# Kernel optimization log

Hardware: AMD Instinct MI355X
Metric: run time of the kernel (lower is better)

Reference implementation:

```python
import jax, jax.numpy as jnp
import numpy as np
from jax import lax

DIM, HF, WF = 768, 14, 8   # h = H, w = W//2 + 1
B, H, W = 128, 14, 14
EPS = 1e-5


def setup_inputs() -> dict:
    key = jax.random.key(0)
    k = jax.random.split(key, 5)
    half = DIM // 2
    return {
        "x": jax.random.normal(k[0], (B, DIM, H, W), dtype=jnp.float32),
        "dw_weight": jax.random.normal(k[1], (half, 1, 3, 3), dtype=jnp.float32) * 0.1,
        "complex_weight": jax.random.normal(k[2], (half, HF, WF, 2), dtype=jnp.float32) * 0.02,
        "proj_weight": jax.random.normal(k[3], (DIM, DIM, 1, 1), dtype=jnp.float32) * 0.02,
        "proj_bias": jnp.zeros((DIM,), dtype=jnp.float32),
        "bn_gamma": jnp.ones((DIM,), dtype=jnp.float32),
        "bn_beta": jnp.zeros((DIM,), dtype=jnp.float32),
    }


def reference(x, dw_weight, complex_weight, proj_weight, proj_bias, bn_gamma, bn_beta):
    half = x.shape[1] // 2
    x1, x2 = x[:, :half], x[:, half:]

    # depthwise 3x3 conv, padding=1, no bias
    x1 = lax.conv_general_dilated(
        x1, dw_weight, window_strides=(1, 1), padding="SAME",
        dimension_numbers=("NCHW", "OIHW", "NCHW"), feature_group_count=half)

    # spectral filter: rfft2 -> complex elementwise multiply -> irfft2 (ortho norm)
    x2_fft = jnp.fft.rfft2(x2, norm="ortho")               # [B, half, H, W//2+1]
    w_fft = complex_weight[..., 0] + 1j * complex_weight[..., 1]  # [half, h, w]
    x2_filt = jnp.fft.irfft2(x2_fft * w_fft, s=(x2.shape[-2], x2.shape[-1]), norm="ortho")

    out = jnp.concatenate((x1, x2_filt), axis=1)           # [B, DIM, H, W]

    # 1x1 projection conv with bias (a GEMM over channels)
    w = proj_weight[:, :, 0, 0]                            # [DIM, DIM]
    out = jnp.einsum("bchw,oc->bohw", out, w) + proj_bias[None, :, None, None]

    # BatchNorm2d, training mode (batch statistics over N,H,W)
    mean = jnp.mean(out, axis=(0, 2, 3), keepdims=True)
    var = jnp.var(out, axis=(0, 2, 3), keepdims=True)
    out = (out - mean) * lax.rsqrt(var + EPS)
    out = out * bn_gamma[None, :, None, None] + bn_beta[None, :, None, None]
    return out
```

## Files before the change

kernel.cpp:

```cpp
#include <hip/hip_runtime.h>

typedef __attribute__((ext_vector_type(8))) __bf16 bf16x8;
typedef __attribute__((ext_vector_type(4))) float f32x4;

#define B_    128
#define DIM_  768
#define HALF_ 384
#define HW_   196
#define NPOS_ (B_*HW_)
#define IMG_  (DIM_*HW_)

__device__ __forceinline__ unsigned short f2bf(float f) {
  unsigned int u = __builtin_bit_cast(unsigned int, f);
  u = (u + 0x7FFFu + ((u >> 16) & 1u)) >> 16;
  return (unsigned short)u;
}

__global__ void k_wspatial(const float* __restrict__ cw, float* __restrict__ wsp) {
  __shared__ float ct[14], st[14];
  const int c = blockIdx.x;
  const int tid = threadIdx.x;
  if (tid < 14) {
    float s, co;
    sincosf(0.44879895051282760549f * (float)tid, &s, &co);
    ct[tid] = co; st[tid] = s;
  }
  __syncthreads();
  const int y = tid / 14, xx = tid % 14;
  float acc = 0.f;
  for (int u = 0; u < 14; ++u) {
    #pragma unroll
    for (int v = 0; v < 8; ++v) {
      int idx = (u * y + v * xx) % 14;
      float wr = cw[(((size_t)c * 14 + u) * 8 + v) * 2 + 0];
      float wi = cw[(((size_t)c * 14 + u) * 8 + v) * 2 + 1];
      float fac = (v == 0 || v == 7) ? 1.f : 2.f;
      acc += fac * (wr * ct[idx] - wi * st[idx]);
    }
  }
  wsp[(size_t)c * 196 + tid] = acc * (1.f / 196.f);
}

__global__ void k_cvtW(const float* __restrict__ pw, unsigned short* __restrict__ Wb) {
  int i = blockIdx.x * 256 + threadIdx.x;
  float4 v = reinterpret_cast<const float4*>(pw)[i];
  unsigned int lo = (unsigned int)f2bf(v.x) | ((unsigned int)f2bf(v.y) << 16);
  unsigned int hi = (unsigned int)f2bf(v.z) | ((unsigned int)f2bf(v.w) << 16);
  reinterpret_cast<uint2*>(Wb)[i] = make_uint2(lo, hi);
}

__global__ __launch_bounds__(256) void k_dwconv(
    const float* __restrict__ x, const float* __restrict__ dww,
    unsigned short* __restrict__ featT) {
  __shared__ __align__(16) float xin[16][196];
  __shared__ float wgt[16][9];
  __shared__ __align__(16) unsigned short outT[196][16];
  const int cgrp = blockIdx.x;
  const int b = blockIdx.y;
  const int c0 = cgrp * 16;
  const int tid = threadIdx.x;

  for (int i = tid; i < 16 * 196; i += 256)
    xin[i / 196][i % 196] = x[(size_t)b * IMG_ + (size_t)(c0 + i / 196) * 196 + (i % 196)];
  if (tid < 144) wgt[tid / 9][tid % 9] = dww[(size_t)c0 * 9 + tid];
  __syncthreads();

  if (tid < 224) {
    const int cc = tid / 14;
    const int y0 = tid % 14;
    float w00 = wgt[cc][0], w01 = wgt[cc][1], w02 = wgt[cc][2];
    float w10 = wgt[cc][3], w11 = wgt[cc][4], w12 = wgt[cc][5];
    float w20 = wgt[cc][6], w21 = wgt[cc][7], w22 = wgt[cc][8];
    #pragma unroll
    for (int xx = 0; xx < 14; ++xx) {
      float acc = 0.f;
      #pragma unroll
      for (int ky = 0; ky < 3; ++ky) {
        int yy = y0 + ky - 1;
        bool yok = (yy >= 0) && (yy <= 13);
        #pragma unroll
        for (int kx = 0; kx < 3; ++kx) {
          int xs = xx + kx - 1;
          if (xs < 0 || xs > 13) continue;
          float wv = (ky == 0) ? (kx == 0 ? w00 : kx == 1 ? w01 : w02)
                   : (ky == 1) ? (kx == 0 ? w10 : kx == 1 ? w11 : w12)
                               : (kx == 0 ? w20 : kx == 1 ? w21 : w22);
          if (yok) acc += xin[cc][yy * 14 + xs] * wv;
        }
      }
      outT[y0 * 14 + xx][cc] = f2bf(acc);
    }
  }
  __syncthreads();
  for (int i = tid; i < 196 * 16; i += 256) {
    int pix = i >> 4, cc = i & 15;
    featT[(size_t)(b * 196 + pix) * DIM_ + (c0 + cc)] = outT[pix][cc];
  }
}

__global__ __launch_bounds__(256) void k_circconv(
    const float* __restrict__ x, const float* __restrict__ wsp,
    unsigned short* __restrict__ featT) {
  __shared__ __align__(16) float xin[16][196];
  __shared__ __align__(16) float wf[16][196];
  __shared__ __align__(16) unsigned short outT[196][16];
  const int cgrp = blockIdx.x;
  const int b = blockIdx.y;
  const int cw0 = cgrp * 16;
  const int c0 = HALF_ + cw0;
  const int tid = threadIdx.x;

  for (int i = tid; i < 16 * 196; i += 256) {
    int cc = i / 196, p = i % 196;
    xin[cc][p] = x[(size_t)b * IMG_ + (size_t)(c0 + cc) * 196 + p];
    wf[cc][p] = wsp[(size_t)(cw0 + cc) * 196 + p];
  }
  __syncthreads();

  if (tid < 224) {
    const int cc = tid / 14;
    const int y0 = tid % 14;
    float outv[14];
    #pragma unroll
    for (int i = 0; i < 14; ++i) outv[i] = 0.f;
    for (int p = 0; p < 14; ++p) {
      int ry = y0 - p; if (ry < 0) ry += 14;
      float xr[14];
      const float2* row2 = reinterpret_cast<const float2*>(&xin[cc][ry * 14]);
      #pragma unroll
      for (int j = 0; j < 7; ++j) { float2 t = row2[j]; xr[2 * j] = t.x; xr[2 * j + 1] = t.y; }
      #pragma unroll
      for (int q = 0; q < 14; ++q) {
        float wv = wf[cc][p * 14 + q];
        #pragma unroll
        for (int xo = 0; xo < 14; ++xo)
          outv[xo] += wv * xr[(xo - q + 14) % 14];
      }
    }
    #pragma unroll
    for (int xo = 0; xo < 14; ++xo) outT[y0 * 14 + xo][cc] = f2bf(outv[xo]);
  }
  __syncthreads();
  for (int i = tid; i < 196 * 16; i += 256) {
    int pix = i >> 4, cc = i & 15;
    featT[(size_t)(b * 196 + pix) * DIM_ + (c0 + cc)] = outT[pix][cc];
  }
}

__global__ __launch_bounds__(256) void k_gemm(
    const unsigned short* __restrict__ Wb, const unsigned short* __restrict__ featT,
    const float* __restrict__ bias, float* __restrict__ y) {
  __shared__ __align__(16) unsigned short As[128 * 64];
  __shared__ __align__(16) unsigned short Bs[128 * 64];

  const int bx = blockIdx.x;
  const int by = blockIdx.y;
  const int tid = threadIdx.x;
  const int lane = tid & 63;
  const int wave = tid >> 6;
  const int wm = wave >> 1;
  const int wn = wave & 1;
  const int o_blk = by * 128;
  const int n_blk = bx * 128;

  f32x4 acc[4][4];
  #pragma unroll
  for (int i = 0; i < 4; ++i)
    #pragma unroll
    for (int j = 0; j < 4; ++j) acc[i][j] = (f32x4)0.0f;

  for (int kt = 0; kt < 768; kt += 64) {
    #pragma unroll
    for (int i = 0; i < 4; ++i) {
      int chunk = i * 256 + tid;
      int r = chunk >> 3;
      int cs = (chunk & 7) * 8;
      uint4 va = *reinterpret_cast<const uint4*>(Wb + (size_t)(o_blk + r) * 768 + kt + cs);
      uint4 vb = *reinterpret_cast<const uint4*>(featT + (size_t)(n_blk + r) * 768 + kt + cs);
      *reinterpret_cast<uint4*>(&As[chunk * 8]) = va;
      *reinterpret_cast<uint4*>(&Bs[chunk * 8]) = vb;
    }
    __syncthreads();
    #pragma unroll
    for (int ks = 0; ks < 64; ks += 32) {
      bf16x8 af[4], bfr[4];
      #pragma unroll
      for (int mi = 0; mi < 4; ++mi) {
        int row = wm * 64 + mi * 16 + (lane & 15);
        int col = ks + (lane >> 4) * 8;
        af[mi] = *reinterpret_cast<const bf16x8*>(&As[row * 64 + col]);
      }
      #pragma unroll
      for (int ni = 0; ni < 4; ++ni) {
        int row = wn * 64 + ni * 16 + (lane & 15);
        int col = ks + (lane >> 4) * 8;
        bfr[ni] = *reinterpret_cast<const bf16x8*>(&Bs[row * 64 + col]);
      }
      #pragma unroll
      for (int mi = 0; mi < 4; ++mi)
        #pragma unroll
        for (int ni = 0; ni < 4; ++ni)
          acc[mi][ni] = __builtin_amdgcn_mfma_f32_16x16x32_bf16(af[mi], bfr[ni], acc[mi][ni], 0, 0, 0);
    }
    __syncthreads();
  }

  const int col_l = lane & 15;
  #pragma unroll
  for (int mi = 0; mi < 4; ++mi) {
    const int o0 = o_blk + wm * 64 + mi * 16 + (lane >> 4) * 4;
    float bs0 = bias[o0], bs1 = bias[o0 + 1], bs2 = bias[o0 + 2], bs3 = bias[o0 + 3];
    #pragma unroll
    for (int ni = 0; ni < 4; ++ni) {
      int n = n_blk + wn * 64 + ni * 16 + col_l;
      int b = n / 196;
      int hw = n % 196;
      size_t base = (size_t)b * IMG_ + (size_t)o0 * 196 + hw;
      y[base +   0] = acc[mi][ni][0] + bs0;
      y[base + 196] = acc[mi][ni][1] + bs1;
      y[base + 392] = acc[mi][ni][2] + bs2;
      y[base + 588] = acc[mi][ni][3] + bs3;
    }
  }
}

__global__ __launch_bounds__(256) void k_bnstats(const float* __restrict__ y,
                                                 float* __restrict__ stats) {
  const int o = blockIdx.x;
  const int tid = threadIdx.x;
  float s = 0.f, s2 = 0.f;
  for (int i = tid; i < NPOS_; i += 256) {
    int b = i / 196, hw = i % 196;
    float v = y[(size_t)b * IMG_ + (size_t)o * 196 + hw];
    s += v; s2 += v * v;
  }
  #pragma unroll
  for (int m = 1; m < 64; m <<= 1) { s += __shfl_xor(s, m); s2 += __shfl_xor(s2, m); }
  __shared__ float rs[4], rs2[4];
  if ((tid & 63) == 0) { rs[tid >> 6] = s; rs2[tid >> 6] = s2; }
  __syncthreads();
  if (tid == 0) {
    float S = rs[0] + rs[1] + rs[2] + rs[3];
    float S2 = rs2[0] + rs2[1] + rs2[2] + rs2[3];
    float mean = S / (float)NPOS_;
    float var = S2 / (float)NPOS_ - mean * mean;
    stats[o] = mean;
    stats[DIM_ + o] = rsqrtf(var + 1e-5f);
  }
}

__global__ void k_bnapply(float* __restrict__ y, const float* __restrict__ stats,
                          const float* __restrict__ gamma, const float* __restrict__ beta) {
  const size_t total4 = (size_t)B_ * DIM_ * HW_ / 4;
  const size_t stride = (size_t)gridDim.x * blockDim.x;
  for (size_t i4 = (size_t)blockIdx.x * blockDim.x + threadIdx.x; i4 < total4; i4 += stride) {
    float4 v = reinterpret_cast<float4*>(y)[i4];
    size_t flat = i4 * 4;
    int o = (int)((flat / 196) % DIM_);
    float g = gamma[o] * stats[DIM_ + o];
    float be = beta[o] - stats[o] * g;
    v.x = v.x * g + be; v.y = v.y * g + be; v.z = v.z * g + be; v.w = v.w * g + be;
    reinterpret_cast<float4*>(y)[i4] = v;
  }
}

extern "C" void kernel_launch(void* const* d_in, const int* in_sizes, int n_in,
                              void* d_out, int out_size, void* d_ws, size_t ws_size,
                              hipStream_t stream) {
  const float* x     = (const float*)d_in[0];
  const float* dww   = (const float*)d_in[1];
  const float* cw    = (const float*)d_in[2];
  const float* pw    = (const float*)d_in[3];
  const float* pb    = (const float*)d_in[4];
  const float* gamma = (const float*)d_in[5];
  const float* beta  = (const float*)d_in[6];
  float* out = (float*)d_out;

  char* wsb = (char*)d_ws;
  unsigned short* featT = (unsigned short*)wsb;
  unsigned short* Wb    = (unsigned short*)(wsb + 38535168);
  float* wsp   = (float*)(wsb + 38535168 + 1179648);
  float* stats = (float*)(wsb + 38535168 + 1179648 + 301056);

  k_wspatial<<<dim3(HALF_), dim3(HW_), 0, stream>>>(cw, wsp);
  k_cvtW<<<dim3(576), dim3(256), 0, stream>>>(pw, Wb);
  k_dwconv<<<dim3(24, B_), dim3(256), 0, stream>>>(x, dww, featT);
  k_circconv<<<dim3(24, B_), dim3(256), 0, stream>>>(x, wsp, featT);
  k_gemm<<<dim3(196, 6), dim3(256), 0, stream>>>(Wb, featT, pb, out);
  k_bnstats<<<dim3(DIM_), dim3(256), 0, stream>>>(out, stats);
  k_bnapply<<<dim3(2048), dim3(256), 0, stream>>>(out, stats, gamma, beta);
}
```

Before: 356.0 us.

## Run circular conv as MFMA GEMM, fuse BN stats into GEMM epilogue

The spectral branch's per-thread scalar circular convolution becomes a per-channel bf16 MFMA matmul. For each channel, a 196x196 circulant matrix built from the spatial filter multiplies the batch-by-pixel input, and a new transpose kernel writes the result back into the channel-last feature buffer. The separate BN statistics pass is removed: the GEMM epilogue reduces sum and sum of squares per channel and accumulates them with atomics, and bnapply derives mean and variance from those sums. GEMM tile loads also switch to direct global-to-LDS loads. This adds bf16 rounding of the spectral inputs, an extra intermediate buffer and transpose pass, and non-deterministic atomic accumulation.

```diff
diff --git a/kernel.cpp b/kernel.cpp
--- a/kernel.cpp
+++ b/kernel.cpp
@@ -10,10 +10,18 @@
 #define NPOS_ (B_*HW_)
 #define IMG_  (DIM_*HW_)
 
+typedef const __attribute__((address_space(1))) void* gas_t;
+typedef __attribute__((address_space(3))) void* las_t;
+
 __device__ __forceinline__ unsigned short f2bf(float f) {
   unsigned int u = __builtin_bit_cast(unsigned int, f);
   u = (u + 0x7FFFu + ((u >> 16) & 1u)) >> 16;
   return (unsigned short)u;
+}
+
+__global__ void k_zero(float* __restrict__ stats) {
+  int i = blockIdx.x * 256 + threadIdx.x;
+  if (i < 2 * DIM_) stats[i] = 0.f;
 }
 
 __global__ void k_wspatial(const float* __restrict__ cw, float* __restrict__ wsp) {
@@ -98,58 +106,114 @@
   }
 }
 
-__global__ __launch_bounds__(256) void k_circconv(
+__global__ __launch_bounds__(256) void k_circmm(
     const float* __restrict__ x, const float* __restrict__ wsp,
-    unsigned short* __restrict__ featT) {
-  __shared__ __align__(16) float xin[16][196];
-  __shared__ __align__(16) float wf[16][196];
-  __shared__ __align__(16) unsigned short outT[196][16];
-  const int cgrp = blockIdx.x;
-  const int b = blockIdx.y;
-  const int cw0 = cgrp * 16;
-  const int c0 = HALF_ + cw0;
-  const int tid = threadIdx.x;
-
-  for (int i = tid; i < 16 * 196; i += 256) {
-    int cc = i / 196, p = i % 196;
-    xin[cc][p] = x[(size_t)b * IMG_ + (size_t)(c0 + cc) * 196 + p];
-    wf[cc][p] = wsp[(size_t)(cw0 + cc) * 196 + p];
+    unsigned short* __restrict__ feat2) {
+  __shared__ __align__(16) unsigned short As[128 * 72];
+  __shared__ __align__(16) unsigned short Bs[208 * 72];
+  const int c = blockIdx.x;
+  const int tid = threadIdx.x;
+  const int lane = tid & 63;
+  const int wv = tid >> 6;
+  const int fr = lane & 15, fg = lane >> 4;
+  const float* xc = x + (size_t)(HALF_ + c) * 196;
+  const float* wspc = wsp + (size_t)c * 196;
+
+  f32x4 acc[2][13];
+  #pragma unroll
+  for (int mi = 0; mi < 2; ++mi)
+    #pragma unroll
+    for (int ni = 0; ni < 13; ++ni) acc[mi][ni] = (f32x4)0.0f;
+
+  for (int kt = 0; kt < 4; ++kt) {
+    for (int i = tid; i < 2048; i += 256) {
+      int b = i >> 4, jj = i & 15;
+      int k = kt * 64 + jj * 4;
+      ushort4 st = {0, 0, 0, 0};
+      if (k < 196) {
+        float4 v = *reinterpret_cast<const float4*>(xc + (size_t)b * IMG_ + k);
+        st.x = f2bf(v.x); st.y = f2bf(v.y); st.z = f2bf(v.z); st.w = f2bf(v.w);
+      }
+      *reinterpret_cast<ushort4*>(&As[b * 72 + jj * 4]) = st;
+    }
+    for (int i = tid; i < 12544; i += 256) {
+      int po = i >> 6, kl = i & 63;
+      int pi = kt * 64 + kl;
+      unsigned short w = 0;
+      if (pi < 196) {
+        int yo = po / 14, xo = po - yo * 14;
+        int yi = pi / 14, xi = pi - yi * 14;
+        int dy = yo - yi; dy += (dy >> 31) & 14;
+        int dx = xo - xi; dx += (dx >> 31) & 14;
+        w = f2bf(wspc[dy * 14 + dx]);
+      }
+      Bs[po * 72 + kl] = w;
+    }
+    __syncthreads();
+    #pragma unroll
+    for (int ks = 0; ks < 64; ks += 32) {
+      bf16x8 a0 = *reinterpret_cast<const bf16x8*>(&As[(wv * 32 + fr) * 72 + ks + fg * 8]);
+      bf16x8 a1 = *reinterpret_cast<const bf16x8*>(&As[(wv * 32 + 16 + fr) * 72 + ks + fg * 8]);
+      #pragma unroll
+      for (int ni = 0; ni < 13; ++ni) {
+        bf16x8 bv = *reinterpret_cast<const bf16x8*>(&Bs[(ni * 16 + fr) * 72 + ks + fg * 8]);
+        acc[0][ni] = __builtin_amdgcn_mfma_f32_16x16x32_bf16(a0, bv, acc[0][ni], 0, 0, 0);
+        acc[1][ni] = __builtin_amdgcn_mfma_f32_16x16x32_bf16(a1, bv, acc[1][ni], 0, 0, 0);
+      }
+    }
+    __syncthreads();
+  }
+
+  unsigned short* f2c = feat2 + (size_t)c * NPOS_;
+  #pragma unroll
+  for (int mi = 0; mi < 2; ++mi) {
+    int b0 = wv * 32 + mi * 16 + fg * 4;
+    #pragma unroll
+    for (int ni = 0; ni < 13; ++ni) {
+      int p = ni * 16 + fr;
+      if (p < 196) {
+        #pragma unroll
+        for (int j = 0; j < 4; ++j)
+          f2c[(size_t)(b0 + j) * 196 + p] = f2bf(acc[mi][ni][j]);
+      }
+    }
+  }
+}
+
+__global__ __launch_bounds__(256) void k_tr(
+    const unsigned short* __restrict__ feat2, unsigned short* __restrict__ featT) {
+  __shared__ __align__(16) unsigned short T2[64 * 264];
+  const int n0 = blockIdx.x * 256;
+  const int c0 = blockIdx.y * 64;
+  const int tid = threadIdx.x;
+
+  #pragma unroll
+  for (int p = 0; p < 8; ++p) {
+    int i = tid + p * 256;
+    int c_l = i >> 5, nj = i & 31;
+    uint4 v = *reinterpret_cast<const uint4*>(feat2 + (size_t)(c0 + c_l) * NPOS_ + n0 + nj * 8);
+    *reinterpret_cast<uint4*>(&T2[c_l * 264 + nj * 8]) = v;
   }
   __syncthreads();
-
-  if (tid < 224) {
-    const int cc = tid / 14;
-    const int y0 = tid % 14;
-    float outv[14];
-    #pragma unroll
-    for (int i = 0; i < 14; ++i) outv[i] = 0.f;
-    for (int p = 0; p < 14; ++p) {
-      int ry = y0 - p; if (ry < 0) ry += 14;
-      float xr[14];
-      const float2* row2 = reinterpret_cast<const float2*>(&xin[cc][ry * 14]);
-      #pragma unroll
-      for (int j = 0; j < 7; ++j) { float2 t = row2[j]; xr[2 * j] = t.x; xr[2 * j + 1] = t.y; }
-      #pragma unroll
-      for (int q = 0; q < 14; ++q) {
-        float wv = wf[cc][p * 14 + q];
-        #pragma unroll
-        for (int xo = 0; xo < 14; ++xo)
-          outv[xo] += wv * xr[(xo - q + 14) % 14];
-      }
-    }
-    #pragma unroll
-    for (int xo = 0; xo < 14; ++xo) outT[y0 * 14 + xo][cc] = f2bf(outv[xo]);
-  }
-  __syncthreads();
-  for (int i = tid; i < 196 * 16; i += 256) {
-    int pix = i >> 4, cc = i & 15;
-    featT[(size_t)(b * 196 + pix) * DIM_ + (c0 + cc)] = outT[pix][cc];
+  #pragma unroll
+  for (int p = 0; p < 8; ++p) {
+    int i = tid + p * 256;
+    int n_l = i >> 3, cj = i & 7;
+    unsigned short vs[8];
+    #pragma unroll
+    for (int k = 0; k < 8; ++k) vs[k] = T2[(cj * 8 + k) * 264 + n_l];
+    uint4 o;
+    o.x = (unsigned int)vs[0] | ((unsigned int)vs[1] << 16);
+    o.y = (unsigned int)vs[2] | ((unsigned int)vs[3] << 16);
+    o.z = (unsigned int)vs[4] | ((unsigned int)vs[5] << 16);
+    o.w = (unsigned int)vs[6] | ((unsigned int)vs[7] << 16);
+    *reinterpret_cast<uint4*>(featT + (size_t)(n0 + n_l) * DIM_ + HALF_ + c0 + cj * 8) = o;
   }
 }
 
 __global__ __launch_bounds__(256) void k_gemm(
     const unsigned short* __restrict__ Wb, const unsigned short* __restrict__ featT,
-    const float* __restrict__ bias, float* __restrict__ y) {
+    const float* __restrict__ bias, float* __restrict__ y, float* __restrict__ stats) {
   __shared__ __align__(16) unsigned short As[128 * 64];
   __shared__ __align__(16) unsigned short Bs[128 * 64];
 
@@ -175,10 +239,12 @@
       int chunk = i * 256 + tid;
       int r = chunk >> 3;
       int cs = (chunk & 7) * 8;
-      uint4 va = *reinterpret_cast<const uint4*>(Wb + (size_t)(o_blk + r) * 768 + kt + cs);
-      uint4 vb = *reinterpret_cast<const uint4*>(featT + (size_t)(n_blk + r) * 768 + kt + cs);
-      *reinterpret_cast<uint4*>(&As[chunk * 8]) = va;
-      *reinterpret_cast<uint4*>(&Bs[chunk * 8]) = vb;
+      __builtin_amdgcn_global_load_lds(
+          (gas_t)(Wb + (size_t)(o_blk + r) * 768 + kt + cs),
+          (las_t)(&As[chunk * 8]), 16, 0, 0);
+      __builtin_amdgcn_global_load_lds(
+          (gas_t)(featT + (size_t)(n_blk + r) * 768 + kt + cs),
+          (las_t)(&Bs[chunk * 8]), 16, 0, 0);
     }
     __syncthreads();
     #pragma unroll
@@ -209,43 +275,32 @@
   #pragma unroll
   for (int mi = 0; mi < 4; ++mi) {
     const int o0 = o_blk + wm * 64 + mi * 16 + (lane >> 4) * 4;
-    float bs0 = bias[o0], bs1 = bias[o0 + 1], bs2 = bias[o0 + 2], bs3 = bias[o0 + 3];
+    float bs[4], sv[4], s2v[4];
+    #pragma unroll
+    for (int j = 0; j < 4; ++j) { bs[j] = bias[o0 + j]; sv[j] = 0.f; s2v[j] = 0.f; }
     #pragma unroll
     for (int ni = 0; ni < 4; ++ni) {
       int n = n_blk + wn * 64 + ni * 16 + col_l;
       int b = n / 196;
       int hw = n % 196;
       size_t base = (size_t)b * IMG_ + (size_t)o0 * 196 + hw;
-      y[base +   0] = acc[mi][ni][0] + bs0;
-      y[base + 196] = acc[mi][ni][1] + bs1;
-      y[base + 392] = acc[mi][ni][2] + bs2;
-      y[base + 588] = acc[mi][ni][3] + bs3;
-    }
-  }
-}
-
-__global__ __launch_bounds__(256) void k_bnstats(const float* __restrict__ y,
-                                                 float* __restrict__ stats) {
-  const int o = blockIdx.x;
-  const int tid = threadIdx.x;
-  float s = 0.f, s2 = 0.f;
-  for (int i = tid; i < NPOS_; i += 256) {
-    int b = i / 196, hw = i % 196;
-    float v = y[(size_t)b * IMG_ + (size_t)o * 196 + hw];
-    s += v; s2 += v * v;
-  }
-  #pragma unroll
-  for (int m = 1; m < 64; m <<= 1) { s += __shfl_xor(s, m); s2 += __shfl_xor(s2, m); }
-  __shared__ float rs[4], rs2[4];
-  if ((tid & 63) == 0) { rs[tid >> 6] = s; rs2[tid >> 6] = s2; }
-  __syncthreads();
-  if (tid == 0) {
-    float S = rs[0] + rs[1] + rs[2] + rs[3];
-    float S2 = rs2[0] + rs2[1] + rs2[2] + rs2[3];
-    float mean = S / (float)NPOS_;
-    float var = S2 / (float)NPOS_ - mean * mean;
-    stats[o] = mean;
-    stats[DIM_ + o] = rsqrtf(var + 1e-5f);
+      #pragma unroll
+      for (int j = 0; j < 4; ++j) {
+        float v = acc[mi][ni][j] + bs[j];
+        y[base + j * 196] = v;
+        sv[j] += v; s2v[j] += v * v;
+      }
+    }
+    #pragma unroll
+    for (int j = 0; j < 4; ++j) {
+      float a = sv[j], q = s2v[j];
+      #pragma unroll
+      for (int m = 1; m < 16; m <<= 1) { a += __shfl_xor(a, m); q += __shfl_xor(q, m); }
+      if (col_l == 0) {
+        atomicAdd(&stats[o0 + j], a);
+        atomicAdd(&stats[DIM_ + o0 + j], q);
+      }
+    }
   }
 }
 
@@ -257,8 +312,10 @@
     float4 v = reinterpret_cast<float4*>(y)[i4];
     size_t flat = i4 * 4;
     int o = (int)((flat / 196) % DIM_);
-    float g = gamma[o] * stats[DIM_ + o];
-    float be = beta[o] - stats[o] * g;
+    float mean = stats[o] * (1.f / (float)NPOS_);
+    float var = stats[DIM_ + o] * (1.f / (float)NPOS_) - mean * mean;
+    float g = gamma[o] * rsqrtf(var + 1e-5f);
+    float be = beta[o] - mean * g;
     v.x = v.x * g + be; v.y = v.y * g + be; v.z = v.z * g + be; v.w = v.w * g + be;
     reinterpret_cast<float4*>(y)[i4] = v;
   }
@@ -279,14 +336,16 @@
   char* wsb = (char*)d_ws;
   unsigned short* featT = (unsigned short*)wsb;
   unsigned short* Wb    = (unsigned short*)(wsb + 38535168);
-  float* wsp   = (float*)(wsb + 38535168 + 1179648);
-  float* stats = (float*)(wsb + 38535168 + 1179648 + 301056);
-
+  float* wsp            = (float*)(wsb + 39714816);
+  unsigned short* feat2 = (unsigned short*)(wsb + 40015872);
+  float* stats          = (float*)(wsb + 59283456);
+
+  k_zero<<<dim3(6), dim3(256), 0, stream>>>(stats);
   k_wspatial<<<dim3(HALF_), dim3(HW_), 0, stream>>>(cw, wsp);
   k_cvtW<<<dim3(576), dim3(256), 0, stream>>>(pw, Wb);
   k_dwconv<<<dim3(24, B_), dim3(256), 0, stream>>>(x, dww, featT);
-  k_circconv<<<dim3(24, B_), dim3(256), 0, stream>>>(x, wsp, featT);
-  k_gemm<<<dim3(196, 6), dim3(256), 0, stream>>>(Wb, featT, pb, out);
-  k_bnstats<<<dim3(DIM_), dim3(256), 0, stream>>>(out, stats);
+  k_circmm<<<dim3(HALF_), dim3(256), 0, stream>>>(x, wsp, feat2);
+  k_tr<<<dim3(98, 6), dim3(256), 0, stream>>>(feat2, featT);
+  k_gemm<<<dim3(196, 6), dim3(256), 0, stream>>>(Wb, featT, pb, out, stats);
   k_bnapply<<<dim3(2048), dim3(256), 0, stream>>>(out, stats, gamma, beta);
 }
```

New measurement: 395.9 us. 11.2% more time.
